# Performance work log

Hardware: AMD Instinct MI355X
Metric: run time of the kernel (lower is better)

## Reference

```python
import jax, jax.numpy as jnp
import numpy as np

N, E, EV, D = 50000, 300000, 100000, 256
BN_EPS = 1e-5


def batchnorm(h, gamma, beta):
    # training-mode BN with batch statistics (biased var, matching torch normalization)
    mu = h.mean(axis=0)
    var = h.var(axis=0)
    return gamma * (h - mu) * jax.lax.rsqrt(var + BN_EPS) + beta


def mlp(h, W1, b1, g1, bt1, W2, b2):
    # Linear -> BN -> ReLU -> (Dropout=identity in eval) -> Linear
    h = h @ W1 + b1
    h = jax.nn.relu(batchnorm(h, g1, bt1))
    return h @ W2 + b2


def gine_conv(x, ei, ea, eps, W1, b1, g1, bt1, W2, b2):
    # message: ReLU(x_src + edge_attr); aggregate: scatter-add at dst; update: MLP((1+eps)*x + aggr)
    m = jax.nn.relu(x[ei[0]] + ea)                       # [E, D]
    aggr = jax.ops.segment_sum(m, ei[1], num_segments=N)  # [N, D]
    return mlp((1.0 + eps) * x + aggr, W1, b1, g1, bt1, W2, b2)


def setup_inputs() -> dict:
    key = jax.random.key(0)
    ks = jax.random.split(key, 16)
    s = 1.0 / np.sqrt(D)
    inp = {
        "x": jax.random.normal(ks[0], (N, D), jnp.float32),
        "edge_index": jax.random.randint(ks[1], (2, E), 0, N, jnp.int64),
        "edge_attr_emb": jax.random.normal(ks[2], (E, D), jnp.float32),
        "v_idx": jax.random.randint(ks[3], (2, EV), 0, N, jnp.int64),
        "v_edge_emb": jax.random.normal(ks[4], (EV, D), jnp.float32),
        # conv_down params
        "eps_down": jnp.zeros((), jnp.float32),
        "W1d": jax.random.normal(ks[5], (D, D), jnp.float32) * s,
        "b1d": jnp.zeros((D,), jnp.float32),
        "g1d": jnp.ones((D,), jnp.float32),
        "bt1d": jnp.zeros((D,), jnp.float32),
        "W2d": jax.random.normal(ks[6], (D, D), jnp.float32) * s,
        "b2d": jnp.zeros((D,), jnp.float32),
        # conv_up params
        "eps_up": jnp.zeros((), jnp.float32),
        "W1u": jax.random.normal(ks[7], (D, D), jnp.float32) * s,
        "b1u": jnp.zeros((D,), jnp.float32),
        "g1u": jnp.ones((D,), jnp.float32),
        "bt1u": jnp.zeros((D,), jnp.float32),
        "W2u": jax.random.normal(ks[8], (D, D), jnp.float32) * s,
        "b2u": jnp.zeros((D,), jnp.float32),
        # final BN + residual scales
        "bn_g": jnp.ones((D,), jnp.float32),
        "bn_b": jnp.zeros((D,), jnp.float32),
        "alpha1": jnp.asarray(1.0, jnp.float32),
        "alpha2": jnp.asarray(0.01, jnp.float32),
    }
    return inp


def reference(x, edge_index, edge_attr_emb, v_idx, v_edge_emb,
              eps_down, W1d, b1d, g1d, bt1d, W2d, b2d,
              eps_up, W1u, b1u, g1u, bt1u, W2u, b2u,
              bn_g, bn_b, alpha1, alpha2):
    h_down = gine_conv(x, edge_index, edge_attr_emb, eps_down, W1d, b1d, g1d, bt1d, W2d, b2d)
    h_up = gine_conv(x, v_idx, v_edge_emb, eps_up, W1u, b1u, g1u, bt1u, W2u, b2u)
    out = x + alpha1 * h_down + alpha2 * h_up
    return jax.nn.relu(batchnorm(out, bn_g, bn_b))
```

## Files before the change

### kernel.cpp

```cpp
#include <hip/hip_runtime.h>
#include <math.h>

#define N_NODES 50000
#define DIM 256
#define NE 300000
#define NEV 100000
#define BM 64
#define BK 64
#define NT 16
#define NSLOT 8
#define GRID_PER ((N_NODES + BM - 1) / BM)

typedef float f32x4 __attribute__((ext_vector_type(4)));
typedef short s16x8 __attribute__((ext_vector_type(8)));

__device__ inline unsigned short f2bf(float f) {
    unsigned u = __float_as_uint(f);
    u += 0x7FFF + ((u >> 16) & 1);
    return (unsigned short)(u >> 16);
}
__device__ inline float bf2f(unsigned short s) {
    return __uint_as_float(((unsigned)s) << 16);
}
__device__ inline int swz(int row, int kg) {
    return row * BK + ((kg ^ (row & 7)) << 3);
}

__global__ __launch_bounds__(256) void prepw_kernel(
    const float* __restrict__ W1d, const float* __restrict__ W2d,
    const float* __restrict__ W1u, const float* __restrict__ W2u,
    unsigned short* __restrict__ Wt)
{
    int b = blockIdx.x;
    int w = b >> 8, n = b & 255, k = threadIdx.x;
    const float* W = (w == 0) ? W1d : (w == 1) ? W2d : (w == 2) ? W1u : W2u;
    Wt[(size_t)w * DIM * DIM + (size_t)n * DIM + k] = f2bf(W[(size_t)k * DIM + n]);
}

__global__ __launch_bounds__(256) void hist2_kernel(
    const int* __restrict__ ei, const int* __restrict__ vi,
    int* __restrict__ degD, int* __restrict__ degU)
{
    int i = blockIdx.x * blockDim.x + threadIdx.x;
    if (i < NE) atomicAdd(&degD[ei[NE + i]], 1);
    else if (i < NE + NEV) { int j = i - NE; atomicAdd(&degU[vi[NEV + j]], 1); }
}

__global__ __launch_bounds__(1024) void scan2_kernel(
    int* __restrict__ offD, int* __restrict__ curD,
    int* __restrict__ offU, int* __restrict__ curU)
{
    int* deg_offsets = (blockIdx.x == 0) ? offD : offU;
    int* cursor      = (blockIdx.x == 0) ? curD : curU;
    int E            = (blockIdx.x == 0) ? NE : NEV;
    __shared__ int part[1024];
    int t = threadIdx.x;
    const int CH = (N_NODES + 1023) / 1024;
    int beg = t * CH;
    int end = min(beg + CH, N_NODES);
    int s = 0;
    for (int i = beg; i < end; i++) s += deg_offsets[i];
    part[t] = s;
    __syncthreads();
    for (int off = 1; off < 1024; off <<= 1) {
        int v = part[t];
        int u = (t >= off) ? part[t - off] : 0;
        __syncthreads();
        part[t] = v + u;
        __syncthreads();
    }
    int run = (t > 0) ? part[t - 1] : 0;
    for (int i = beg; i < end; i++) {
        int dv = deg_offsets[i];
        deg_offsets[i] = run;
        cursor[i] = run;
        run += dv;
    }
    if (t == 1023) deg_offsets[N_NODES] = E;
}

__global__ __launch_bounds__(256) void fill2_kernel(
    const int* __restrict__ ei, const int* __restrict__ vi,
    int* __restrict__ curD, int* __restrict__ curU,
    int2* __restrict__ pairsD, int2* __restrict__ pairsU)
{
    int i = blockIdx.x * blockDim.x + threadIdx.x;
    if (i < NE) {
        int s = ei[i], d = ei[NE + i];
        int pos = atomicAdd(&curD[d], 1);
        pairsD[pos] = make_int2(i, s);
    } else if (i < NE + NEV) {
        int j = i - NE;
        int s = vi[j], d = vi[NEV + j];
        int pos = atomicAdd(&curU[d], 1);
        pairsU[pos] = make_int2(j, s);
    }
}

__device__ inline f32x4 ld4(const float* p) { return *(const f32x4*)p; }
__device__ inline f32x4 ldnt4(const float* p) {
    return __builtin_nontemporal_load((const f32x4*)p);
}
__device__ inline void acc_relu(f32x4& acc, f32x4 a, f32x4 b) {
    acc.x += fmaxf(a.x + b.x, 0.f);
    acc.y += fmaxf(a.y + b.y, 0.f);
    acc.z += fmaxf(a.z + b.z, 0.f);
    acc.w += fmaxf(a.w + b.w, 0.f);
}

__global__ __launch_bounds__(256) void gather2_kernel(
    const float* __restrict__ x, const float* __restrict__ ea,
    const float* __restrict__ vea,
    const int* __restrict__ offD, const int2* __restrict__ pairsD,
    const int* __restrict__ offU, const int2* __restrict__ pairsU,
    const float* __restrict__ epsd, const float* __restrict__ epsu,
    unsigned short* __restrict__ hD, unsigned short* __restrict__ hU)
{
    int wid = blockIdx.x * (blockDim.x >> 6) + (threadIdx.x >> 6);
    int lane = threadIdx.x & 63;
    if (wid >= 2 * N_NODES) return;
    bool down = wid < N_NODES;
    int node = down ? wid : wid - N_NODES;
    const int* off      = down ? offD   : offU;
    const int2* pairs   = down ? pairsD : pairsU;
    const float* eat    = down ? ea     : vea;
    unsigned short* h   = down ? hD     : hU;
    float epsv = 1.0f + (down ? epsd[0] : epsu[0]);

    int beg = off[node], end = off[node + 1];
    f32x4 acc = {0.f, 0.f, 0.f, 0.f};
    int cofs = lane * 4;
    int p = beg;
    for (; p + 3 < end; p += 4) {
        int2 q0 = pairs[p], q1 = pairs[p + 1], q2 = pairs[p + 2], q3 = pairs[p + 3];
        f32x4 a0 = ld4(x + (size_t)q0.y * DIM + cofs);
        f32x4 b0 = ldnt4(eat + (size_t)q0.x * DIM + cofs);
        f32x4 a1 = ld4(x + (size_t)q1.y * DIM + cofs);
        f32x4 b1 = ldnt4(eat + (size_t)q1.x * DIM + cofs);
        f32x4 a2 = ld4(x + (size_t)q2.y * DIM + cofs);
        f32x4 b2 = ldnt4(eat + (size_t)q2.x * DIM + cofs);
        f32x4 a3 = ld4(x + (size_t)q3.y * DIM + cofs);
        f32x4 b3 = ldnt4(eat + (size_t)q3.x * DIM + cofs);
        acc_relu(acc, a0, b0);
        acc_relu(acc, a1, b1);
        acc_relu(acc, a2, b2);
        acc_relu(acc, a3, b3);
    }
    for (; p + 1 < end; p += 2) {
        int2 q0 = pairs[p], q1 = pairs[p + 1];
        f32x4 a0 = ld4(x + (size_t)q0.y * DIM + cofs);
        f32x4 b0 = ldnt4(eat + (size_t)q0.x * DIM + cofs);
        f32x4 a1 = ld4(x + (size_t)q1.y * DIM + cofs);
        f32x4 b1 = ldnt4(eat + (size_t)q1.x * DIM + cofs);
        acc_relu(acc, a0, b0);
        acc_relu(acc, a1, b1);
    }
    if (p < end) {
        int2 q0 = pairs[p];
        f32x4 a0 = ld4(x + (size_t)q0.y * DIM + cofs);
        f32x4 b0 = ldnt4(eat + (size_t)q0.x * DIM + cofs);
        acc_relu(acc, a0, b0);
    }
    f32x4 xv = ld4(x + (size_t)node * DIM + cofs);
    acc.x = fmaf(epsv, xv.x, acc.x);
    acc.y = fmaf(epsv, xv.y, acc.y);
    acc.z = fmaf(epsv, xv.z, acc.z);
    acc.w = fmaf(epsv, xv.w, acc.w);
    ushort4 pk;
    pk.x = f2bf(acc.x); pk.y = f2bf(acc.y);
    pk.z = f2bf(acc.z); pk.w = f2bf(acc.w);
    *(ushort4*)(h + (size_t)node * DIM + cofs) = pk;
}

__global__ __launch_bounds__(256) void scatter_kernel(
    const float* __restrict__ x, const float* __restrict__ ea,
    const int* __restrict__ idx, int E, float* __restrict__ buf)
{
    int wid = blockIdx.x * (blockDim.x >> 6) + (threadIdx.x >> 6);
    int lane = threadIdx.x & 63;
    if (wid >= E) return;
    int s = idx[wid];
    int d = idx[E + wid];
    float4 a = ((const float4*)(x + (size_t)s * DIM))[lane];
    float4 b = ((const float4*)(ea + (size_t)wid * DIM))[lane];
    float* dst = buf + (size_t)d * DIM + lane * 4;
    atomicAdd(dst + 0, fmaxf(a.x + b.x, 0.f));
    atomicAdd(dst + 1, fmaxf(a.y + b.y, 0.f));
    atomicAdd(dst + 2, fmaxf(a.z + b.z, 0.f));
    atomicAdd(dst + 3, fmaxf(a.w + b.w, 0.f));
}

__global__ __launch_bounds__(256) void conv_kernel(
    const float* __restrict__ x, const float* __restrict__ aggr,
    const float* __restrict__ eps_p, unsigned short* __restrict__ h)
{
    float epsv = 1.0f + eps_p[0];
    int i = blockIdx.x * blockDim.x + threadIdx.x;
    const int total = N_NODES * (DIM / 4);
    for (int f = i; f < total; f += gridDim.x * blockDim.x) {
        float4 xv = ((const float4*)x)[f];
        float4 av = ((const float4*)aggr)[f];
        ushort4 pk;
        pk.x = f2bf(fmaf(epsv, xv.x, av.x));
        pk.y = f2bf(fmaf(epsv, xv.y, av.y));
        pk.z = f2bf(fmaf(epsv, xv.z, av.z));
        pk.w = f2bf(fmaf(epsv, xv.w, av.w));
        ((ushort4*)h)[f] = pk;
    }
}

__global__ __launch_bounds__(256) void gemm1_both(
    const unsigned short* __restrict__ hD, const unsigned short* __restrict__ hU,
    const unsigned short* __restrict__ Wt1d, const unsigned short* __restrict__ Wt1u,
    const float* __restrict__ b1d, const float* __restrict__ b1u,
    unsigned short* __restrict__ t1D, unsigned short* __restrict__ t1U,
    float* __restrict__ sumD, float* __restrict__ sqD,
    float* __restrict__ sumU, float* __restrict__ sqU)
{
    __shared__ unsigned short As[BM * BK];
    __shared__ unsigned short Bs[DIM * BK];
    __shared__ float sLds[4 * DIM];
    __shared__ float qLds[4 * DIM];
    int blk = blockIdx.x;
    bool down = blk < GRID_PER;
    int bb = down ? blk : blk - GRID_PER;
    const unsigned short* h  = down ? hD   : hU;
    const unsigned short* Wt = down ? Wt1d : Wt1u;
    const float* bias        = down ? b1d  : b1u;
    unsigned short* t1       = down ? t1D  : t1U;
    float* ssum              = down ? sumD : sumU;
    float* ssq               = down ? sqD  : sqU;

    int t = threadIdx.x;
    int w = t >> 6, l = t & 63, lrow = l & 15, kgrp = l >> 4;
    int row0 = bb * BM;

    f32x4 acc[NT];
    #pragma unroll
    for (int nt = 0; nt < NT; ++nt) acc[nt] = (f32x4){0.f, 0.f, 0.f, 0.f};

    for (int k0 = 0; k0 < DIM; k0 += BK) {
        __syncthreads();
        #pragma unroll
        for (int it = 0; it < 2; ++it) {
            int g = it * 256 + t, row = g >> 3, kg = g & 7;
            int gr = row0 + row;
            s16x8 v = {0, 0, 0, 0, 0, 0, 0, 0};
            if (gr < N_NODES)
                v = *(const s16x8*)&h[(size_t)gr * DIM + k0 + kg * 8];
            *(s16x8*)&As[swz(row, kg)] = v;
        }
        #pragma unroll
        for (int it = 0; it < 8; ++it) {
            int g = it * 256 + t, row = g >> 3, kg = g & 7;
            s16x8 v = *(const s16x8*)&Wt[(size_t)row * DIM + k0 + kg * 8];
            *(s16x8*)&Bs[swz(row, kg)] = v;
        }
        __syncthreads();
        int arow = w * 16 + lrow;
        s16x8 af0 = *(const s16x8*)&As[swz(arow, kgrp)];
        s16x8 af1 = *(const s16x8*)&As[swz(arow, 4 + kgrp)];
        #pragma unroll
        for (int nt = 0; nt < NT; ++nt) {
            int col = nt * 16 + lrow;
            s16x8 bf0 = *(const s16x8*)&Bs[swz(col, kgrp)];
            s16x8 bf1 = *(const s16x8*)&Bs[swz(col, 4 + kgrp)];
            acc[nt] = __builtin_amdgcn_mfma_f32_16x16x32_bf16(af0, bf0, acc[nt], 0, 0, 0);
            acc[nt] = __builtin_amdgcn_mfma_f32_16x16x32_bf16(af1, bf1, acc[nt], 0, 0, 0);
        }
    }
    #pragma unroll
    for (int nt = 0; nt < NT; ++nt) {
        int col = nt * 16 + lrow;
        float bv = bias[col];
        float s = 0.f, q = 0.f;
        #pragma unroll
        for (int r = 0; r < 4; ++r) {
            int grow = row0 + w * 16 + kgrp * 4 + r;
            if (grow < N_NODES) {
                float v = acc[nt][r] + bv;
                t1[(size_t)grow * DIM + col] = f2bf(v);
                s += v; q += v * v;
            }
        }
        s += __shfl_xor(s, 16); q += __shfl_xor(q, 16);
        s += __shfl_xor(s, 32); q += __shfl_xor(q, 32);
        if (kgrp == 0) { sLds[w * DIM + col] = s; qLds[w * DIM + col] = q; }
    }
    __syncthreads();
    {
        float s = sLds[t] + sLds[DIM + t] + sLds[2 * DIM + t] + sLds[3 * DIM + t];
        float q = qLds[t] + qLds[DIM + t] + qLds[2 * DIM + t] + qLds[3 * DIM + t];
        int slot = bb & (NSLOT - 1);
        atomicAdd(&ssum[slot * DIM + t], s);
        atomicAdd(&ssq[slot * DIM + t], q);
    }
}

__global__ __launch_bounds__(256) void gemm2_mfma(
    const unsigned short* __restrict__ t1, const float* __restrict__ scale,
    const float* __restrict__ shift, const unsigned short* __restrict__ Wt,
    const float* __restrict__ bias, const float* __restrict__ base,
    const float* __restrict__ alpha_p, float* __restrict__ out, int do_stats,
    float* __restrict__ ssum, float* __restrict__ ssq)
{
    __shared__ unsigned short As[BM * BK];
    __shared__ unsigned short Bs[DIM * BK];
    __shared__ float sLds[4 * DIM];
    __shared__ float qLds[4 * DIM];
    int t = threadIdx.x;
    int w = t >> 6, l = t & 63, lrow = l & 15, kgrp = l >> 4;
    int row0 = blockIdx.x * BM;

    f32x4 acc[NT];
    #pragma unroll
    for (int nt = 0; nt < NT; ++nt) acc[nt] = (f32x4){0.f, 0.f, 0.f, 0.f};

    for (int k0 = 0; k0 < DIM; k0 += BK) {
        __syncthreads();
        #pragma unroll
        for (int it = 0; it < 2; ++it) {
            int g = it * 256 + t, row = g >> 3, kg = g & 7;
            int gr = row0 + row;
            s16x8 pack = {0, 0, 0, 0, 0, 0, 0, 0};
            if (gr < N_NODES) {
                s16x8 tv = *(const s16x8*)(t1 + (size_t)gr * DIM + k0 + kg * 8);
                const float4* scp = (const float4*)(scale + k0 + kg * 8);
                const float4* shp = (const float4*)(shift + k0 + kg * 8);
                float4 s0 = scp[0], s1 = scp[1], h0 = shp[0], h1 = shp[1];
                pack[0] = f2bf(fmaxf(fmaf(bf2f((unsigned short)tv[0]), s0.x, h0.x), 0.f));
                pack[1] = f2bf(fmaxf(fmaf(bf2f((unsigned short)tv[1]), s0.y, h0.y), 0.f));
                pack[2] = f2bf(fmaxf(fmaf(bf2f((unsigned short)tv[2]), s0.z, h0.z), 0.f));
                pack[3] = f2bf(fmaxf(fmaf(bf2f((unsigned short)tv[3]), s0.w, h0.w), 0.f));
                pack[4] = f2bf(fmaxf(fmaf(bf2f((unsigned short)tv[4]), s1.x, h1.x), 0.f));
                pack[5] = f2bf(fmaxf(fmaf(bf2f((unsigned short)tv[5]), s1.y, h1.y), 0.f));
                pack[6] = f2bf(fmaxf(fmaf(bf2f((unsigned short)tv[6]), s1.z, h1.z), 0.f));
                pack[7] = f2bf(fmaxf(fmaf(bf2f((unsigned short)tv[7]), s1.w, h1.w), 0.f));
            }
            *(s16x8*)&As[swz(row, kg)] = pack;
        }
        #pragma unroll
        for (int it = 0; it < 8; ++it) {
            int g = it * 256 + t, row = g >> 3, kg = g & 7;
            s16x8 v = *(const s16x8*)&Wt[(size_t)row * DIM + k0 + kg * 8];
            *(s16x8*)&Bs[swz(row, kg)] = v;
        }
        __syncthreads();
        int arow = w * 16 + lrow;
        s16x8 af0 = *(const s16x8*)&As[swz(arow, kgrp)];
        s16x8 af1 = *(const s16x8*)&As[swz(arow, 4 + kgrp)];
        #pragma unroll
        for (int nt = 0; nt < NT; ++nt) {
            int col = nt * 16 + lrow;
            s16x8 bf0 = *(const s16x8*)&Bs[swz(col, kgrp)];
            s16x8 bf1 = *(const s16x8*)&Bs[swz(col, 4 + kgrp)];
            acc[nt] = __builtin_amdgcn_mfma_f32_16x16x32_bf16(af0, bf0, acc[nt], 0, 0, 0);
            acc[nt] = __builtin_amdgcn_mfma_f32_16x16x32_bf16(af1, bf1, acc[nt], 0, 0, 0);
        }
    }
    float alphav = alpha_p[0];
    #pragma unroll
    for (int nt = 0; nt < NT; ++nt) {
        int col = nt * 16 + lrow;
        float bv = bias[col];
        float s = 0.f, q = 0.f;
        #pragma unroll
        for (int r = 0; r < 4; ++r) {
            int grow = row0 + w * 16 + kgrp * 4 + r;
            if (grow < N_NODES) {
                size_t o = (size_t)grow * DIM + col;
                float v = fmaf(alphav, acc[nt][r] + bv, base[o]);
                out[o] = v;
                s += v; q += v * v;
            }
        }
        if (do_stats) {
            s += __shfl_xor(s, 16); q += __shfl_xor(q, 16);
            s += __shfl_xor(s, 32); q += __shfl_xor(q, 32);
            if (kgrp == 0) { sLds[w * DIM + col] = s; qLds[w * DIM + col] = q; }
        }
    }
    if (do_stats) {
        __syncthreads();
        float s = sLds[t] + sLds[DIM + t] + sLds[2 * DIM + t] + sLds[3 * DIM + t];
        float q = qLds[t] + qLds[DIM + t] + qLds[2 * DIM + t] + qLds[3 * DIM + t];
        int slot = blockIdx.x & (NSLOT - 1);
        atomicAdd(&ssum[slot * DIM + t], s);
        atomicAdd(&ssq[slot * DIM + t], q);
    }
}

__device__ inline void bn_finalize(
    const float* ssum, const float* ssq, const float* g, const float* b,
    float* scale, float* shift, int c)
{
    float s = 0.f, q = 0.f;
    #pragma unroll
    for (int k = 0; k < NSLOT; ++k) { s += ssum[k * DIM + c]; q += ssq[k * DIM + c]; }
    const float invN = 1.0f / (float)N_NODES;
    float mu = s * invN;
    float var = q * invN - mu * mu;
    float sc = g[c] * rsqrtf(var + 1e-5f);
    scale[c] = sc;
    shift[c] = b[c] - mu * sc;
}

__global__ void finalize2_kernel(
    const float* __restrict__ sumD, const float* __restrict__ sqD,
    const float* __restrict__ g1d, const float* __restrict__ bt1d,
    float* __restrict__ scD, float* __restrict__ shD,
    const float* __restrict__ sumU, const float* __restrict__ sqU,
    const float* __restrict__ g1u, const float* __restrict__ bt1u,
    float* __restrict__ scU, float* __restrict__ shU)
{
    int t = threadIdx.x;
    int c = t & (DIM - 1);
    if (t < DIM) bn_finalize(sumD, sqD, g1d, bt1d, scD, shD, c);
    else         bn_finalize(sumU, sqU, g1u, bt1u, scU, shU, c);
}

__global__ void finalize_kernel(
    const float* __restrict__ ssum, const float* __restrict__ ssq,
    const float* __restrict__ g, const float* __restrict__ b,
    float* __restrict__ scale, float* __restrict__ shift)
{
    bn_finalize(ssum, ssq, g, b, scale, shift, threadIdx.x);
}

__global__ __launch_bounds__(256) void bnrelu_kernel(
    float* __restrict__ out, const float* __restrict__ scale,
    const float* __restrict__ shift)
{
    int idx = blockIdx.x * blockDim.x + threadIdx.x;
    const int total = N_NODES * (DIM / 4);
    for (int f = idx; f < total; f += gridDim.x * blockDim.x) {
        float4 v = ((float4*)out)[f];
        int c = (f * 4) & (DIM - 1);
        float4 sc = *(const float4*)(scale + c);
        float4 sh = *(const float4*)(shift + c);
        v.x = fmaxf(v.x * sc.x + sh.x, 0.0f);
        v.y = fmaxf(v.y * sc.y + sh.y, 0.0f);
        v.z = fmaxf(v.z * sc.z + sh.z, 0.0f);
        v.w = fmaxf(v.w * sc.w + sh.w, 0.0f);
        ((float4*)out)[f] = v;
    }
}

extern "C" void kernel_launch(void* const* d_in, const int* in_sizes, int n_in,
                              void* d_out, int out_size, void* d_ws, size_t ws_size,
                              hipStream_t stream)
{
    const float* x    = (const float*)d_in[0];
    const int*   ei   = (const int*)  d_in[1];
    const float* ea   = (const float*)d_in[2];
    const int*   vi   = (const int*)  d_in[3];
    const float* vea  = (const float*)d_in[4];
    const float* epsd = (const float*)d_in[5];
    const float* W1d  = (const float*)d_in[6];
    const float* b1d  = (const float*)d_in[7];
    const float* g1d  = (const float*)d_in[8];
    const float* bt1d = (const float*)d_in[9];
    const float* W2d  = (const float*)d_in[10];
    const float* b2d  = (const float*)d_in[11];
    const float* epsu = (const float*)d_in[12];
    const float* W1u  = (const float*)d_in[13];
    const float* b1u  = (const float*)d_in[14];
    const float* g1u  = (const float*)d_in[15];
    const float* bt1u = (const float*)d_in[16];
    const float* W2u  = (const float*)d_in[17];
    const float* b2u  = (const float*)d_in[18];
    const float* bng  = (const float*)d_in[19];
    const float* bnb  = (const float*)d_in[20];
    const float* a1   = (const float*)d_in[21];
    const float* a2   = (const float*)d_in[22];

    float* out = (float*)d_out;

    char* p = (char*)d_ws;
    unsigned short* hD  = (unsigned short*)p;  p += (size_t)N_NODES * DIM * 2;
    unsigned short* hU  = (unsigned short*)p;  p += (size_t)N_NODES * DIM * 2;
    unsigned short* t1D = (unsigned short*)p;  p += (size_t)N_NODES * DIM * 2;
    unsigned short* t1U = (unsigned short*)p;  p += (size_t)N_NODES * DIM * 2;
    unsigned short* Wt  = (unsigned short*)p;  p += (size_t)4 * DIM * DIM * 2;
    float* scD = (float*)p;                    p += DIM * 4;
    float* shD = (float*)p;                    p += DIM * 4;
    float* scU = (float*)p;                    p += DIM * 4;
    float* shU = (float*)p;                    p += DIM * 4;
    char* zero_base = p;
    float* stats = (float*)p;                  p += (size_t)6 * NSLOT * DIM * 4;
    int* offD = (int*)p;                       p += (size_t)(N_NODES + 1) * 4;
    int* offU = (int*)p;                       p += (size_t)(N_NODES + 1) * 4;
    size_t zero_bytes = (size_t)(p - zero_base);
    int* curD = (int*)p;                       p += (size_t)N_NODES * 4;
    int* curU = (int*)p;                       p += (size_t)N_NODES * 4;
    char* union_base = p;
    int2* pairsD = (int2*)p;                   p += (size_t)NE * 8;
    int2* pairsU = (int2*)p;                   p += (size_t)NEV * 8;
    size_t need_csr = (size_t)(p - (char*)d_ws);
    float* aggr = (float*)union_base;
    size_t need_fb = (size_t)(union_base - (char*)d_ws) + (size_t)N_NODES * DIM * 4;
    bool use_csr = ws_size >= need_csr;

    float* sumD = stats;
    float* sqD  = stats + 1 * NSLOT * DIM;
    float* sumU = stats + 2 * NSLOT * DIM;
    float* sqU  = stats + 3 * NSLOT * DIM;
    float* sumF = stats + 4 * NSLOT * DIM;
    float* sqF  = stats + 5 * NSLOT * DIM;

    unsigned short* Wt1d = Wt;
    unsigned short* Wt2d = Wt + 1 * (size_t)DIM * DIM;
    unsigned short* Wt1u = Wt + 2 * (size_t)DIM * DIM;
    unsigned short* Wt2u = Wt + 3 * (size_t)DIM * DIM;

    hipMemsetAsync(zero_base, 0, zero_bytes, stream);
    prepw_kernel<<<4 * DIM, 256, 0, stream>>>(W1d, W2d, W1u, W2u, Wt);

    if (use_csr) {
        hist2_kernel<<<(NE + NEV + 255) / 256, 256, 0, stream>>>(ei, vi, offD, offU);
        scan2_kernel<<<2, 1024, 0, stream>>>(offD, curD, offU, curU);
        fill2_kernel<<<(NE + NEV + 255) / 256, 256, 0, stream>>>(
            ei, vi, curD, curU, pairsD, pairsU);
        gather2_kernel<<<(2 * N_NODES + 3) / 4, 256, 0, stream>>>(
            x, ea, vea, offD, pairsD, offU, pairsU, epsd, epsu, hD, hU);
    } else if (ws_size >= need_fb) {
        hipMemsetAsync(aggr, 0, (size_t)N_NODES * DIM * 4, stream);
        scatter_kernel<<<(NE + 3) / 4, 256, 0, stream>>>(x, ea, ei, NE, aggr);
        conv_kernel<<<2048, 256, 0, stream>>>(x, aggr, epsd, hD);
        hipMemsetAsync(aggr, 0, (size_t)N_NODES * DIM * 4, stream);
        scatter_kernel<<<(NEV + 3) / 4, 256, 0, stream>>>(x, vea, vi, NEV, aggr);
        conv_kernel<<<2048, 256, 0, stream>>>(x, aggr, epsu, hU);
    }

    gemm1_both<<<2 * GRID_PER, 256, 0, stream>>>(
        hD, hU, Wt1d, Wt1u, b1d, b1u, t1D, t1U, sumD, sqD, sumU, sqU);
    finalize2_kernel<<<1, 2 * DIM, 0, stream>>>(
        sumD, sqD, g1d, bt1d, scD, shD, sumU, sqU, g1u, bt1u, scU, shU);

    gemm2_mfma<<<GRID_PER, 256, 0, stream>>>(t1D, scD, shD, Wt2d, b2d, x, a1, out,
                                             0, sumF, sqF);
    gemm2_mfma<<<GRID_PER, 256, 0, stream>>>(t1U, scU, shU, Wt2u, b2u, out, a2, out,
                                             1, sumF, sqF);
    finalize_kernel<<<1, 256, 0, stream>>>(sumF, sqF, bng, bnb, scD, shD);
    bnrelu_kernel<<<2048, 256, 0, stream>>>(out, scD, shD);
}
```

Baseline: 508.2 us.

## Split gather across two warps, retile MFMA GEMMs, merge gemm2 launches with combine pass

```diff
diff --git a/kernel.cpp b/kernel.cpp
--- a/kernel.cpp
+++ b/kernel.cpp
@@ -7,7 +7,6 @@
 #define NEV 100000
 #define BM 64
 #define BK 64
-#define NT 16
 #define NSLOT 8
 #define GRID_PER ((N_NODES + BM - 1) / BM)
 
@@ -116,11 +115,14 @@
     const float* __restrict__ epsd, const float* __restrict__ epsu,
     unsigned short* __restrict__ hD, unsigned short* __restrict__ hU)
 {
-    int wid = blockIdx.x * (blockDim.x >> 6) + (threadIdx.x >> 6);
+    __shared__ f32x4 part[2][64];
+    int warp = threadIdx.x >> 6;
     int lane = threadIdx.x & 63;
-    if (wid >= 2 * N_NODES) return;
-    bool down = wid < N_NODES;
-    int node = down ? wid : wid - N_NODES;
+    int slotn = warp >> 1;
+    int half = warp & 1;
+    int nidx = blockIdx.x * 2 + slotn;
+    bool down = nidx < N_NODES;
+    int node = down ? nidx : nidx - N_NODES;
     const int* off      = down ? offD   : offU;
     const int2* pairs   = down ? pairsD : pairsU;
     const float* eat    = down ? ea     : vea;
@@ -130,24 +132,9 @@
     int beg = off[node], end = off[node + 1];
     f32x4 acc = {0.f, 0.f, 0.f, 0.f};
     int cofs = lane * 4;
-    int p = beg;
-    for (; p + 3 < end; p += 4) {
-        int2 q0 = pairs[p], q1 = pairs[p + 1], q2 = pairs[p + 2], q3 = pairs[p + 3];
-        f32x4 a0 = ld4(x + (size_t)q0.y * DIM + cofs);
-        f32x4 b0 = ldnt4(eat + (size_t)q0.x * DIM + cofs);
-        f32x4 a1 = ld4(x + (size_t)q1.y * DIM + cofs);
-        f32x4 b1 = ldnt4(eat + (size_t)q1.x * DIM + cofs);
-        f32x4 a2 = ld4(x + (size_t)q2.y * DIM + cofs);
-        f32x4 b2 = ldnt4(eat + (size_t)q2.x * DIM + cofs);
-        f32x4 a3 = ld4(x + (size_t)q3.y * DIM + cofs);
-        f32x4 b3 = ldnt4(eat + (size_t)q3.x * DIM + cofs);
-        acc_relu(acc, a0, b0);
-        acc_relu(acc, a1, b1);
-        acc_relu(acc, a2, b2);
-        acc_relu(acc, a3, b3);
-    }
-    for (; p + 1 < end; p += 2) {
-        int2 q0 = pairs[p], q1 = pairs[p + 1];
+    int p = beg + half;
+    for (; p + 2 < end; p += 4) {
+        int2 q0 = pairs[p], q1 = pairs[p + 2];
         f32x4 a0 = ld4(x + (size_t)q0.y * DIM + cofs);
         f32x4 b0 = ldnt4(eat + (size_t)q0.x * DIM + cofs);
         f32x4 a1 = ld4(x + (size_t)q1.y * DIM + cofs);
@@ -161,15 +148,21 @@
         f32x4 b0 = ldnt4(eat + (size_t)q0.x * DIM + cofs);
         acc_relu(acc, a0, b0);
     }
-    f32x4 xv = ld4(x + (size_t)node * DIM + cofs);
-    acc.x = fmaf(epsv, xv.x, acc.x);
-    acc.y = fmaf(epsv, xv.y, acc.y);
-    acc.z = fmaf(epsv, xv.z, acc.z);
-    acc.w = fmaf(epsv, xv.w, acc.w);
-    ushort4 pk;
-    pk.x = f2bf(acc.x); pk.y = f2bf(acc.y);
-    pk.z = f2bf(acc.z); pk.w = f2bf(acc.w);
-    *(ushort4*)(h + (size_t)node * DIM + cofs) = pk;
+    if (half == 1) part[slotn][lane] = acc;
+    __syncthreads();
+    if (half == 0) {
+        f32x4 o = part[slotn][lane];
+        acc.x += o.x; acc.y += o.y; acc.z += o.z; acc.w += o.w;
+        f32x4 xv = ld4(x + (size_t)node * DIM + cofs);
+        acc.x = fmaf(epsv, xv.x, acc.x);
+        acc.y = fmaf(epsv, xv.y, acc.y);
+        acc.z = fmaf(epsv, xv.z, acc.z);
+        acc.w = fmaf(epsv, xv.w, acc.w);
+        ushort4 pk;
+        pk.x = f2bf(acc.x); pk.y = f2bf(acc.y);
+        pk.z = f2bf(acc.z); pk.w = f2bf(acc.w);
+        *(ushort4*)(h + (size_t)node * DIM + cofs) = pk;
+    }
 }
 
 __global__ __launch_bounds__(256) void scatter_kernel(
@@ -219,8 +212,6 @@
 {
     __shared__ unsigned short As[BM * BK];
     __shared__ unsigned short Bs[DIM * BK];
-    __shared__ float sLds[4 * DIM];
-    __shared__ float qLds[4 * DIM];
     int blk = blockIdx.x;
     bool down = blk < GRID_PER;
     int bb = down ? blk : blk - GRID_PER;
@@ -235,9 +226,9 @@
     int w = t >> 6, l = t & 63, lrow = l & 15, kgrp = l >> 4;
     int row0 = bb * BM;
 
-    f32x4 acc[NT];
+    f32x4 acc[16];
     #pragma unroll
-    for (int nt = 0; nt < NT; ++nt) acc[nt] = (f32x4){0.f, 0.f, 0.f, 0.f};
+    for (int i = 0; i < 16; ++i) acc[i] = (f32x4){0.f, 0.f, 0.f, 0.f};
 
     for (int k0 = 0; k0 < DIM; k0 += BK) {
         __syncthreads();
@@ -257,64 +248,79 @@
             *(s16x8*)&Bs[swz(row, kg)] = v;
         }
         __syncthreads();
-        int arow = w * 16 + lrow;
-        s16x8 af0 = *(const s16x8*)&As[swz(arow, kgrp)];
-        s16x8 af1 = *(const s16x8*)&As[swz(arow, 4 + kgrp)];
-        #pragma unroll
-        for (int nt = 0; nt < NT; ++nt) {
-            int col = nt * 16 + lrow;
-            s16x8 bf0 = *(const s16x8*)&Bs[swz(col, kgrp)];
-            s16x8 bf1 = *(const s16x8*)&Bs[swz(col, 4 + kgrp)];
-            acc[nt] = __builtin_amdgcn_mfma_f32_16x16x32_bf16(af0, bf0, acc[nt], 0, 0, 0);
-            acc[nt] = __builtin_amdgcn_mfma_f32_16x16x32_bf16(af1, bf1, acc[nt], 0, 0, 0);
-        }
-    }
+        #pragma unroll
+        for (int kk = 0; kk < 2; ++kk) {
+            s16x8 af[4], bf[4];
+            #pragma unroll
+            for (int mi = 0; mi < 4; ++mi)
+                af[mi] = *(const s16x8*)&As[swz(mi * 16 + lrow, kk * 4 + kgrp)];
+            #pragma unroll
+            for (int ni = 0; ni < 4; ++ni)
+                bf[ni] = *(const s16x8*)&Bs[swz(w * 64 + ni * 16 + lrow, kk * 4 + kgrp)];
+            #pragma unroll
+            for (int mi = 0; mi < 4; ++mi)
+                #pragma unroll
+                for (int ni = 0; ni < 4; ++ni)
+                    acc[mi * 4 + ni] = __builtin_amdgcn_mfma_f32_16x16x32_bf16(
+                        af[mi], bf[ni], acc[mi * 4 + ni], 0, 0, 0);
+        }
+    }
+    int slot = bb & (NSLOT - 1);
     #pragma unroll
-    for (int nt = 0; nt < NT; ++nt) {
-        int col = nt * 16 + lrow;
+    for (int ni = 0; ni < 4; ++ni) {
+        int col = w * 64 + ni * 16 + lrow;
         float bv = bias[col];
         float s = 0.f, q = 0.f;
         #pragma unroll
-        for (int r = 0; r < 4; ++r) {
-            int grow = row0 + w * 16 + kgrp * 4 + r;
-            if (grow < N_NODES) {
-                float v = acc[nt][r] + bv;
-                t1[(size_t)grow * DIM + col] = f2bf(v);
-                s += v; q += v * v;
+        for (int mi = 0; mi < 4; ++mi) {
+            #pragma unroll
+            for (int r = 0; r < 4; ++r) {
+                int grow = row0 + mi * 16 + kgrp * 4 + r;
+                if (grow < N_NODES) {
+                    float v = acc[mi * 4 + ni][r] + bv;
+                    t1[(size_t)grow * DIM + col] = f2bf(v);
+                    s += v; q += v * v;
+                }
             }
         }
         s += __shfl_xor(s, 16); q += __shfl_xor(q, 16);
         s += __shfl_xor(s, 32); q += __shfl_xor(q, 32);
-        if (kgrp == 0) { sLds[w * DIM + col] = s; qLds[w * DIM + col] = q; }
-    }
-    __syncthreads();
-    {
-        float s = sLds[t] + sLds[DIM + t] + sLds[2 * DIM + t] + sLds[3 * DIM + t];
-        float q = qLds[t] + qLds[DIM + t] + qLds[2 * DIM + t] + qLds[3 * DIM + t];
-        int slot = bb & (NSLOT - 1);
-        atomicAdd(&ssum[slot * DIM + t], s);
-        atomicAdd(&ssq[slot * DIM + t], q);
-    }
-}
-
-__global__ __launch_bounds__(256) void gemm2_mfma(
-    const unsigned short* __restrict__ t1, const float* __restrict__ scale,
-    const float* __restrict__ shift, const unsigned short* __restrict__ Wt,
-    const float* __restrict__ bias, const float* __restrict__ base,
-    const float* __restrict__ alpha_p, float* __restrict__ out, int do_stats,
-    float* __restrict__ ssum, float* __restrict__ ssq)
+        if (kgrp == 0) {
+            atomicAdd(&ssum[slot * DIM + col], s);
+            atomicAdd(&ssq[slot * DIM + col], q);
+        }
+    }
+}
+
+__global__ __launch_bounds__(256) void gemm2_both(
+    const unsigned short* __restrict__ t1D, const unsigned short* __restrict__ t1U,
+    const float* __restrict__ scD, const float* __restrict__ shD,
+    const float* __restrict__ scU, const float* __restrict__ shU,
+    const unsigned short* __restrict__ Wt2d, const unsigned short* __restrict__ Wt2u,
+    const float* __restrict__ b2d, const float* __restrict__ b2u,
+    const float* __restrict__ a1, const float* __restrict__ a2,
+    float* __restrict__ C1, float* __restrict__ C2)
 {
     __shared__ unsigned short As[BM * BK];
     __shared__ unsigned short Bs[DIM * BK];
-    __shared__ float sLds[4 * DIM];
-    __shared__ float qLds[4 * DIM];
+    int blk = blockIdx.x;
+    bool down = blk < GRID_PER;
+    int bb = down ? blk : blk - GRID_PER;
+    const unsigned short* t1 = down ? t1D  : t1U;
+    const float* scale       = down ? scD  : scU;
+    const float* shift       = down ? shD  : shU;
+    const unsigned short* Wt = down ? Wt2d : Wt2u;
+    const float* bias        = down ? b2d  : b2u;
+    float alphav             = down ? a1[0] : a2[0];
+    float* C                 = down ? C1   : C2;
+
     int t = threadIdx.x;
     int w = t >> 6, l = t & 63, lrow = l & 15, kgrp = l >> 4;
-    int row0 = blockIdx.x * BM;
-
-    f32x4 acc[NT];
+    int row0 = bb * BM;
+
+    f32x4 acc[16];
     #pragma unroll
-    for (int nt = 0; nt < NT; ++nt) acc[nt] = (f32x4){0.f, 0.f, 0.f, 0.f};
+    for (int i = 0; i < 16; ++i) acc[i] = (f32x4){0.f, 0.f, 0.f, 0.f};
 
     for (int k0 = 0; k0 < DIM; k0 += BK) {
         __syncthreads();
@@ -346,47 +352,71 @@
             *(s16x8*)&Bs[swz(row, kg)] = v;
         }
         __syncthreads();
-        int arow = w * 16 + lrow;
-        s16x8 af0 = *(const s16x8*)&As[swz(arow, kgrp)];
-        s16x8 af1 = *(const s16x8*)&As[swz(arow, 4 + kgrp)];
-        #pragma unroll
-        for (int nt = 0; nt < NT; ++nt) {
-            int col = nt * 16 + lrow;
-            s16x8 bf0 = *(const s16x8*)&Bs[swz(col, kgrp)];
-            s16x8 bf1 = *(const s16x8*)&Bs[swz(col, 4 + kgrp)];
-            acc[nt] = __builtin_amdgcn_mfma_f32_16x16x32_bf16(af0, bf0, acc[nt], 0, 0, 0);
-            acc[nt] = __builtin_amdgcn_mfma_f32_16x16x32_bf16(af1, bf1, acc[nt], 0, 0, 0);
-        }
-    }
-    float alphav = alpha_p[0];
+        #pragma unroll
+        for (int kk = 0; kk < 2; ++kk) {
+            s16x8 af[4], bf[4];
+            #pragma unroll
+            for (int mi = 0; mi < 4; ++mi)
+                af[mi] = *(const s16x8*)&As[swz(mi * 16 + lrow, kk * 4 + kgrp)];
+            #pragma unroll
+            for (int ni = 0; ni < 4; ++ni)
+                bf[ni] = *(const s16x8*)&Bs[swz(w * 64 + ni * 16 + lrow, kk * 4 + kgrp)];
+            #pragma unroll
+            for (int mi = 0; mi < 4; ++mi)
+                #pragma unroll
+                for (int ni = 0; ni < 4; ++ni)
+                    acc[mi * 4 + ni] = __builtin_amdgcn_mfma_f32_16x16x32_bf16(
+                        af[mi], bf[ni], acc[mi * 4 + ni], 0, 0, 0);
+        }
+    }
     #pragma unroll
-    for (int nt = 0; nt < NT; ++nt) {
-        int col = nt * 16 + lrow;
+    for (int ni = 0; ni < 4; ++ni) {
+        int col = w * 64 + ni * 16 + lrow;
         float bv = bias[col];
-        float s = 0.f, q = 0.f;
-        #pragma unroll
-        for (int r = 0; r < 4; ++r) {
-            int grow = row0 + w * 16 + kgrp * 4 + r;
-            if (grow < N_NODES) {
-                size_t o = (size_t)grow * DIM + col;
-                float v = fmaf(alphav, acc[nt][r] + bv, base[o]);
-                out[o] = v;
-                s += v; q += v * v;
+        #pragma unroll
+        for (int mi = 0; mi < 4; ++mi) {
+            #pragma unroll
+            for (int r = 0; r < 4; ++r) {
+                int grow = row0 + mi * 16 + kgrp * 4 + r;
+                if (grow < N_NODES)
+                    C[(size_t)grow * DIM + col] = alphav * (acc[mi * 4 + ni][r] + bv);
             }
         }
-        if (do_stats) {
-            s += __shfl_xor(s, 16); q += __shfl_xor(q, 16);
-            s += __shfl_xor(s, 32); q += __shfl_xor(q, 32);
-            if (kgrp == 0) { sLds[w * DIM + col] = s; qLds[w * DIM + col] = q; }
-        }
-    }
-    if (do_stats) {
-        __syncthreads();
-        float s = sLds[t] + sLds[DIM + t] + sLds[2 * DIM + t] + sLds[3 * DIM + t];
-        float q = qLds[t] + qLds[DIM + t] + qLds[2 * DIM + t] + qLds[3 * DIM + t];
+    }
+}
+
+__global__ __launch_bounds__(256) void combine_kernel(
+    const float* __restrict__ x, const float* __restrict__ C1,
+    const float* __restrict__ C2, float* __restrict__ out,
+    float* __restrict__ ssum, float* __restrict__ ssq)
+{
+    __shared__ f32x4 sS[4][64];
+    __shared__ f32x4 sQ[4][64];
+    int t = threadIdx.x;
+    int cq = t & 63, rg = t >> 6;
+    f32x4 s = {0.f, 0.f, 0.f, 0.f}, q = {0.f, 0.f, 0.f, 0.f};
+    const int rowstep = gridDim.x * 4;
+    for (int row = blockIdx.x * 4 + rg; row < N_NODES; row += rowstep) {
+        size_t f = (size_t)row * 64 + cq;
+        f32x4 v = ((const f32x4*)x)[f] + ((const f32x4*)C1)[f] + ((const f32x4*)C2)[f];
+        ((f32x4*)out)[f] = v;
+        s += v; q += v * v;
+    }
+    sS[rg][cq] = s; sQ[rg][cq] = q;
+    __syncthreads();
+    if (rg == 0) {
+        s = sS[0][cq] + sS[1][cq] + sS[2][cq] + sS[3][cq];
+        q = sQ[0][cq] + sQ[1][cq] + sQ[2][cq] + sQ[3][cq];
         int slot = blockIdx.x & (NSLOT - 1);
-        atomicAdd(&ssum[slot * DIM + t], s);
-        atomicAdd(&ssq[slot * DIM + t], q);
+        int c = cq * 4;
+        atomicAdd(&ssum[slot * DIM + c + 0], s.x);
+        atomicAdd(&ssum[slot * DIM + c + 1], s.y);
+        atomicAdd(&ssum[slot * DIM + c + 2], s.z);
+        atomicAdd(&ssum[slot * DIM + c + 3], s.w);
+        atomicAdd(&ssq[slot * DIM + c + 0], q.x);
+        atomicAdd(&ssq[slot * DIM + c + 1], q.y);
+        atomicAdd(&ssq[slot * DIM + c + 2], q.z);
+        atomicAdd(&ssq[slot * DIM + c + 3], q.w);
     }
 }
 
@@ -482,6 +512,8 @@
     unsigned short* t1D = (unsigned short*)p;  p += (size_t)N_NODES * DIM * 2;
     unsigned short* t1U = (unsigned short*)p;  p += (size_t)N_NODES * DIM * 2;
     unsigned short* Wt  = (unsigned short*)p;  p += (size_t)4 * DIM * DIM * 2;
+    float* C1 = (float*)p;                     p += (size_t)N_NODES * DIM * 4;
+    float* C2 = (float*)p;                     p += (size_t)N_NODES * DIM * 4;
     float* scD = (float*)p;                    p += DIM * 4;
     float* shD = (float*)p;                    p += DIM * 4;
     float* scU = (float*)p;                    p += DIM * 4;
@@ -521,7 +553,7 @@
         scan2_kernel<<<2, 1024, 0, stream>>>(offD, curD, offU, curU);
         fill2_kernel<<<(NE + NEV + 255) / 256, 256, 0, stream>>>(
             ei, vi, curD, curU, pairsD, pairsU);
-        gather2_kernel<<<(2 * N_NODES + 3) / 4, 256, 0, stream>>>(
+        gather2_kernel<<<N_NODES, 256, 0, stream>>>(
             x, ea, vea, offD, pairsD, offU, pairsU, epsd, epsu, hD, hU);
     } else if (ws_size >= need_fb) {
         hipMemsetAsync(aggr, 0, (size_t)N_NODES * DIM * 4, stream);
@@ -537,10 +569,10 @@
     finalize2_kernel<<<1, 2 * DIM, 0, stream>>>(
         sumD, sqD, g1d, bt1d, scD, shD, sumU, sqU, g1u, bt1u, scU, shU);
 
-    gemm2_mfma<<<GRID_PER, 256, 0, stream>>>(t1D, scD, shD, Wt2d, b2d, x, a1, out,
-                                             0, sumF, sqF);
-    gemm2_mfma<<<GRID_PER, 256, 0, stream>>>(t1U, scU, shU, Wt2u, b2u, out, a2, out,
-                                             1, sumF, sqF);
+    gemm2_both<<<2 * GRID_PER, 256, 0, stream>>>(
+        t1D, t1U, scD, shD, scU, shU, Wt2d, Wt2u, b2d, b2u, a1, a2, C1, C2);
+
+    combine_kernel<<<1024, 256, 0, stream>>>(x, C1, C2, out, sumF, sqF);
     finalize_kernel<<<1, 256, 0, stream>>>(sumF, sqF, bng, bnb, scD, shD);
     bnrelu_kernel<<<2048, 256, 0, stream>>>(out, scD, shD);
 }
```

Measured after the change: 487.2 us. 4.1% less time.
